# Optimization experiments

Hardware: AMD Instinct MI355X
Metric: run time of the kernel (lower is better)

The kernel has to match this reference:

```python
import jax, jax.numpy as jnp
import numpy as np

EPS = 1e-5


def layer_norm(x, g, b):
    mu = jnp.mean(x, axis=-1, keepdims=True)
    var = jnp.var(x, axis=-1, keepdims=True)
    return (x - mu) * jax.lax.rsqrt(var + EPS) * g + b


def setup_inputs() -> dict:
    key = jax.random.key(0)
    ks = jax.random.split(key, 10)
    B, N, D, H, DFF = 4, 2048, 384, 6, 2048
    s = lambda fan: 1.0 / np.sqrt(fan)
    return {
        "x": jax.random.normal(ks[0], (B, N, D), dtype=jnp.float32),
        "norm_g": jnp.ones((D,), jnp.float32),
        "norm_b": jnp.zeros((D,), jnp.float32),
        "w_qkv": jax.random.uniform(ks[1], (D, 3 * D), jnp.float32, -s(D), s(D)),
        "b_qkv": jax.random.uniform(ks[2], (3 * D,), jnp.float32, -s(D), s(D)),
        "w1": jax.random.uniform(ks[3], (D, DFF), jnp.float32, -s(D), s(D)),
        "b1": jax.random.uniform(ks[4], (DFF,), jnp.float32, -s(D), s(D)),
        "w2": jax.random.uniform(ks[5], (DFF, D), jnp.float32, -s(DFF), s(DFF)),
        "b2": jax.random.uniform(ks[6], (D,), jnp.float32, -s(DFF), s(DFF)),
    }


def reference(x, norm_g, norm_b, w_qkv, b_qkv, w1, b1, w2, b2):
    H = 6
    B, N, D = x.shape
    hd = D // H
    scale = hd ** -0.5

    # --- attention (pre-norm, shared LayerNorm params) ---
    out = layer_norm(x, norm_g, norm_b)
    qkv = out @ w_qkv + b_qkv                     # [B, N, 3D]
    q, k, v = jnp.split(qkv, 3, axis=-1)
    to_heads = lambda t: t.reshape(B, N, H, hd).transpose(0, 2, 1, 3)  # b h n d
    q, k, v = to_heads(q), to_heads(k), to_heads(v)
    scores = jnp.einsum('bhid,bhjd->bhij', q, k) * scale
    attn = jax.nn.softmax(scores, axis=-1)        # dropout is identity in eval
    att = jnp.einsum('bhij,bhjd->bhid', attn, v)  # [B, H, N, hd]
    att = att.transpose(0, 2, 1, 3).reshape(B, N, D)
    x2 = x + att

    # --- MLP (same shared LayerNorm) ---
    y = layer_norm(x2, norm_g, norm_b)
    h = jax.nn.gelu(y @ w1 + b1, approximate=False)  # torch F.gelu exact
    mlp = h @ w2 + b2
    return x2 + mlp
```

## Files before the change

### kernel.cpp

```cpp
#include <hip/hip_runtime.h>
#include <cstdint>
#include <cstddef>

#define DEV static __device__ __forceinline__

typedef __attribute__((ext_vector_type(8))) short short8;
typedef __attribute__((ext_vector_type(4))) float f32x4;
typedef __attribute__((ext_vector_type(4))) unsigned short u16x4;
typedef __attribute__((ext_vector_type(2))) unsigned short u16x2;

constexpr int kB = 4, kN = 2048, kD = 384, kH = 6, kDFF = 2048;
constexpr int kM = kB * kN;
constexpr int kBH = kB * kH;
constexpr float kQPre = 0.18033688011112042f;

DEV float exp2fast(float f) { return __builtin_amdgcn_exp2f(f); }

DEV unsigned short f2b(float f) {
  union { float fp; uint32_t u; } v; v.fp = f;
  return (unsigned short)((v.u + 0x7fffu + ((v.u >> 16) & 1u)) >> 16);
}

DEV void gload16(const unsigned short* g, unsigned short* l) {
  __builtin_amdgcn_global_load_lds(
      (const __attribute__((address_space(1))) unsigned int*)g,
      (__attribute__((address_space(3))) unsigned int*)l, 16, 0, 0);
}

DEV float gelu_fast(float x) {
  float t = exp2fast(x * (2.3022081f + 0.1029432f * x * x));
  return x - x * __builtin_amdgcn_rcpf(t + 1.0f);
}

__global__ __launch_bounds__(256) void k_transpose3(
    const float* __restrict__ wqkv, unsigned short* __restrict__ wqkvT,
    const float* __restrict__ w1,   unsigned short* __restrict__ w1T,
    const float* __restrict__ w2,   unsigned short* __restrict__ w2T) {
  __shared__ unsigned short t[64][66];
  int idx = blockIdx.x;
  const float* w; unsigned short* wT; int K, Nn, nbk;
  if (idx < 108)      { w = wqkv; wT = wqkvT; K = 384;  Nn = 1152; nbk = 6; }
  else if (idx < 300) { w = w1;   wT = w1T;   K = 384;  Nn = 2048; nbk = 6;  idx -= 108; }
  else                { w = w2;   wT = w2T;   K = 2048; Nn = 384;  nbk = 32; idx -= 300; }
  const int bk = idx % nbk, bn = idx / nbk;
  const int k0 = bk << 6, n0 = bn << 6;
  const int tid = threadIdx.x;
  const int cl = tid & 63, rw = tid >> 6;
#pragma unroll
  for (int it = 0; it < 16; ++it) {
    int kk = it * 4 + rw;
    t[cl][kk] = f2b(w[(size_t)(k0 + kk) * Nn + n0 + cl]);
  }
  __syncthreads();
  const int kq = (tid & 15) << 2;
  const int nr = tid >> 4;
#pragma unroll
  for (int it = 0; it < 4; ++it) {
    int nn = it * 16 + nr;
    u16x4 v;
    v[0] = t[nn][kq]; v[1] = t[nn][kq + 1]; v[2] = t[nn][kq + 2]; v[3] = t[nn][kq + 3];
    *(u16x4*)&wT[(size_t)(n0 + nn) * K + k0 + kq] = v;
  }
}

__global__ __launch_bounds__(256) void k_layernorm(
    const float* __restrict__ x, const float* __restrict__ g,
    const float* __restrict__ bta, unsigned short* __restrict__ y) {
  int row  = blockIdx.x * 4 + (threadIdx.x >> 6);
  int lane = threadIdx.x & 63;
  const float* xr = x + (size_t)row * kD;
  float4 a = *(const float4*)(xr + lane * 4);
  float2 c = *(const float2*)(xr + 256 + lane * 2);
  float s  = a.x + a.y + a.z + a.w + c.x + c.y;
  float ss = a.x*a.x + a.y*a.y + a.z*a.z + a.w*a.w + c.x*c.x + c.y*c.y;
#pragma unroll
  for (int m = 1; m < 64; m <<= 1) {
    s  += __shfl_xor(s,  m, 64);
    ss += __shfl_xor(ss, m, 64);
  }
  float mean = s * (1.0f / kD);
  float var  = ss * (1.0f / kD) - mean * mean;
  float r = rsqrtf(var + 1e-5f);
  float4 g4 = *(const float4*)(g + lane * 4);
  float2 g2 = *(const float2*)(g + 256 + lane * 2);
  float4 b4 = *(const float4*)(bta + lane * 4);
  float2 b2 = *(const float2*)(bta + 256 + lane * 2);
  unsigned short* yr = y + (size_t)row * kD;
  u16x4 o4;
  o4[0] = f2b((a.x - mean) * r * g4.x + b4.x);
  o4[1] = f2b((a.y - mean) * r * g4.y + b4.y);
  o4[2] = f2b((a.z - mean) * r * g4.z + b4.z);
  o4[3] = f2b((a.w - mean) * r * g4.w + b4.w);
  *(u16x4*)(yr + lane * 4) = o4;
  u16x2 o2;
  o2[0] = f2b((c.x - mean) * r * g2.x + b2.x);
  o2[1] = f2b((c.y - mean) * r * g2.y + b2.y);
  *(u16x2*)(yr + 256 + lane * 2) = o2;
}

template <int MODE, int TM>
__global__ __launch_bounds__(256) void k_gemm(
    const unsigned short* __restrict__ A, const unsigned short* __restrict__ Bt,
    const float* __restrict__ bias, int K, int Nn, int nbm,
    unsigned short* __restrict__ oq, unsigned short* __restrict__ okk,
    unsigned short* __restrict__ ov, unsigned short* __restrict__ oh,
    const float* __restrict__ res, float* __restrict__ out) {
  constexpr int MI = (TM + 31) / 32;
  __shared__ unsigned short lA[2][TM * 32];
  __shared__ unsigned short lB[2][128 * 32];
  const int tid = threadIdx.x, wid = tid >> 6, lane = tid & 63;
  const int bm = blockIdx.x % nbm, bn = blockIdx.x / nbm;
  const int m0 = bm * TM, n0 = bn * 128;
  const int wr = wid >> 1, wc = wid & 1;
  const int wmo = wr * (TM >> 1);
  const int lr16 = lane & 15, lq = lane >> 4;
  const int gsw = ((lr16 >> 1) & 3) << 3;

  f32x4 acc[MI][4];
#pragma unroll
  for (int i = 0; i < MI; i++)
#pragma unroll
    for (int j = 0; j < 4; j++) acc[i][j] = f32x4{0.f, 0.f, 0.f, 0.f};

  const int srow = (lane >> 2);
  const int scc  = (lane & 3) << 3;

  auto stage = [&](int buf, int k0) {
    if constexpr (TM >= 64) {
#pragma unroll
      for (int p = 0; p < TM / 64; p++) {
        int row = ((wid + (p << 2)) << 4) + srow;
        int sl  = ((lane & 3) ^ ((row >> 1) & 3)) << 3;
        gload16(A + (size_t)(m0 + row) * K + k0 + sl, &lA[buf][(row << 5) + scc]);
      }
    } else {
      if (tid < TM * 4) {
        int row = tid >> 2;
        int sl  = ((tid & 3) ^ ((row >> 1) & 3)) << 3;
        gload16(A + (size_t)(m0 + row) * K + k0 + sl,
                &lA[buf][(row << 5) + ((tid & 3) << 3)]);
      }
    }
#pragma unroll
    for (int p = 0; p < 2; p++) {
      int row = ((wid + (p << 2)) << 4) + srow;
      int sl  = ((lane & 3) ^ ((row >> 1) & 3)) << 3;
      gload16(Bt + (size_t)(n0 + row) * K + k0 + sl, &lB[buf][(row << 5) + scc]);
    }
  };

  stage(0, 0);

  const int nkt = K >> 5;
  for (int kt = 0; kt < nkt; ++kt) {
    const int cur = kt & 1;
    __syncthreads();
    if (kt + 1 < nkt) stage(cur ^ 1, (kt + 1) << 5);
    short8 af[MI], bf[4];
#pragma unroll
    for (int i = 0; i < MI; i++)
      af[i] = *(const short8*)&lA[cur][(wmo + (i << 4) + lr16) * 32 + ((lq << 3) ^ gsw)];
#pragma unroll
    for (int j = 0; j < 4; j++)
      bf[j] = *(const short8*)&lB[cur][((wc << 6) + (j << 4) + lr16) * 32 + ((lq << 3) ^ gsw)];
#pragma unroll
    for (int i = 0; i < MI; i++)
#pragma unroll
      for (int j = 0; j < 4; j++)
        acc[i][j] = __builtin_amdgcn_mfma_f32_16x16x32_bf16(af[i], bf[j], acc[i][j], 0, 0, 0);
  }

#pragma unroll
  for (int i = 0; i < MI; i++) {
    int mbase = m0 + wmo + (i << 4) + (lq << 2);
#pragma unroll
    for (int j = 0; j < 4; j++) {
      int col = n0 + (wc << 6) + (j << 4) + lr16;
      float bv = bias[col];
#pragma unroll
      for (int rr = 0; rr < 4; ++rr) {
        float cvl = acc[i][j][rr] + bv;
        int m = mbase + rr;
        if (MODE == 0) {
          int bI = m >> 11, nI = m & 2047;
          if (col < 384) {
            int hh = col >> 6, dd = col & 63;
            oq[(((size_t)bI * kH + hh) * kN + nI) * 64 + dd] = f2b(cvl * kQPre);
          } else if (col < 768) {
            int c2 = col - 384; int hh = c2 >> 6, dd = c2 & 63;
            okk[(((size_t)bI * kH + hh) * kN + nI) * 64 + dd] = f2b(cvl);
          } else {
            int c2 = col - 768; int hh = c2 >> 6, dd = c2 & 63;
            ov[(((size_t)bI * kH + hh) * 64 + dd) * kN + nI] = f2b(cvl);
          }
        } else if (MODE == 1) {
          oh[(size_t)m * kDFF + col] = f2b(gelu_fast(cvl));
        } else {
          size_t idx = (size_t)m * kD + col;
          out[idx] = res[idx] + cvl;
        }
      }
    }
  }
}

__global__ __launch_bounds__(256) void k_attn(
    const unsigned short* __restrict__ Q, const unsigned short* __restrict__ Kg,
    const unsigned short* __restrict__ Vt, const float* __restrict__ x,
    float* __restrict__ x2) {
  __shared__ unsigned short lK[2][64 * 64];
  __shared__ unsigned short lV[2][64 * 64];
  __shared__ unsigned short lP[4][16 * 64];
  const int tid = threadIdx.x, wid = tid >> 6, lane = tid & 63;
  const int swz = (blockIdx.x & 7) * (gridDim.x >> 3) + (blockIdx.x >> 3);
  const int bh = swz >> 5, qt = swz & 31;
  const int b = bh / kH, h = bh - b * kH;
  const unsigned short* Qp = Q  + (size_t)bh * kN * 64;
  const unsigned short* Kp = Kg + (size_t)bh * kN * 64;
  const unsigned short* Vp = Vt + (size_t)bh * 64 * kN;
  const int lr16 = lane & 15, lq = lane >> 4;
  const int q0w = qt * 64 + wid * 16;
  const int rsw = (lr16 & 7) << 3;

  const int sr  = ((wid << 3) + (lane >> 3));
  const int scc = (lane & 7) << 3;

  short8 qf[2];
#pragma unroll
  for (int ks = 0; ks < 2; ++ks)
    qf[ks] = *(const short8*)(Qp + (size_t)(q0w + lr16) * 64 + ks * 32 + lq * 8);

  const short8 ones = {0x3F80, 0x3F80, 0x3F80, 0x3F80, 0x3F80, 0x3F80, 0x3F80, 0x3F80};
  f32x4 o[4], o_l;
#pragma unroll
  for (int df = 0; df < 4; ++df) o[df] = f32x4{0.f, 0.f, 0.f, 0.f};
  o_l = f32x4{0.f, 0.f, 0.f, 0.f};

  auto stage = [&](int buf, int t) {
#pragma unroll
    for (int p = 0; p < 2; p++) {
      int r = sr + (p << 5);
      int sl = ((lane & 7) ^ (r & 7)) << 3;
      gload16(Kp + (size_t)(t * 64 + r) * 64 + sl, &lK[buf][(r << 6) + scc]);
      gload16(Vp + (size_t)r * kN + t * 64 + sl,   &lV[buf][(r << 6) + scc]);
    }
  };

  stage(0, 0);

  constexpr int kNT = kN / 64;
  for (int t = 0; t < kNT; ++t) {
    const int cur = t & 1;
    __syncthreads();
    if (t + 1 < kNT) stage(cur ^ 1, t + 1);

    f32x4 s4[4];
#pragma unroll
    for (int j = 0; j < 4; j++) {
      s4[j] = f32x4{0.f, 0.f, 0.f, 0.f};
#pragma unroll
      for (int ks = 0; ks < 2; ks++) {
        short8 kf = *(const short8*)&lK[cur][((j << 4) + lr16) * 64 + ((ks * 32 + (lq << 3)) ^ rsw)];
        s4[j] = __builtin_amdgcn_mfma_f32_16x16x32_bf16(kf, qf[ks], s4[j], 0, 0, 0);
      }
    }

#pragma unroll
    for (int j = 0; j < 4; j++) {
      float p0 = exp2fast(s4[j][0]);
      float p1 = exp2fast(s4[j][1]);
      float p2 = exp2fast(s4[j][2]);
      float p3 = exp2fast(s4[j][3]);
      uint32_t w0, w1;
      asm("v_cvt_pk_bf16_f32 %0, %1, %2" : "=v"(w0) : "v"(p0), "v"(p1));
      asm("v_cvt_pk_bf16_f32 %0, %1, %2" : "=v"(w1) : "v"(p2), "v"(p3));
      int kvb = (j << 4) + (lq << 2);
      uint2 wv; wv.x = w0; wv.y = w1;
      *(uint2*)&lP[wid][(lr16 << 6) + (kvb ^ rsw)] = wv;
    }

    short8 pa[2];
#pragma unroll
    for (int ks = 0; ks < 2; ks++)
      pa[ks] = *(const short8*)&lP[wid][(lr16 << 6) + ((ks * 32 + (lq << 3)) ^ rsw)];
#pragma unroll
    for (int ks = 0; ks < 2; ks++)
      o_l = __builtin_amdgcn_mfma_f32_16x16x32_bf16(pa[ks], ones, o_l, 0, 0, 0);
#pragma unroll
    for (int df = 0; df < 4; df++) {
#pragma unroll
      for (int ks = 0; ks < 2; ks++) {
        short8 vf = *(const short8*)&lV[cur][((df << 4) + lr16) * 64 + ((ks * 32 + (lq << 3)) ^ rsw)];
        o[df] = __builtin_amdgcn_mfma_f32_16x16x32_bf16(pa[ks], vf, o[df], 0, 0, 0);
      }
    }
  }

  float inv[4];
#pragma unroll
  for (int rr = 0; rr < 4; rr++) inv[rr] = __builtin_amdgcn_rcpf(o_l[rr]);
#pragma unroll
  for (int df = 0; df < 4; df++)
#pragma unroll
    for (int rr = 0; rr < 4; rr++) {
      int row  = q0w + (lq << 2) + rr;
      int colD = h * 64 + (df << 4) + lr16;
      size_t idx = ((size_t)(b * kN + row)) * kD + colD;
      x2[idx] = x[idx] + o[df][rr] * inv[rr];
    }
}

extern "C" void kernel_launch(void* const* d_in, const int* in_sizes, int n_in,
                              void* d_out, int out_size, void* d_ws, size_t ws_size,
                              hipStream_t stream) {
  const float* x    = (const float*)d_in[0];
  const float* ng   = (const float*)d_in[1];
  const float* nb   = (const float*)d_in[2];
  const float* wqkv = (const float*)d_in[3];
  const float* bqkv = (const float*)d_in[4];
  const float* w1   = (const float*)d_in[5];
  const float* b1   = (const float*)d_in[6];
  const float* w2   = (const float*)d_in[7];
  const float* b2   = (const float*)d_in[8];
  float* out = (float*)d_out;

  char* p = (char*)d_ws;
  auto take = [&](size_t bytes) -> char* {
    char* r = p; p += (bytes + 255) & ~(size_t)255; return r;
  };
  unsigned short* y     = (unsigned short*)take((size_t)kM * kD * 2);
  unsigned short* wqkvT = (unsigned short*)take((size_t)3 * kD * kD * 2);
  unsigned short* w1T   = (unsigned short*)take((size_t)kDFF * kD * 2);
  unsigned short* w2T   = (unsigned short*)take((size_t)kD * kDFF * 2);
  unsigned short* Qw    = (unsigned short*)take((size_t)kM * kD * 2);
  unsigned short* Kw    = (unsigned short*)take((size_t)kM * kD * 2);
  unsigned short* Vtw   = (unsigned short*)take((size_t)kM * kD * 2);
  float*          x2    = (float*)take((size_t)kM * kD * 4);
  unsigned short* hbuf  = (unsigned short*)take((size_t)kM * kDFF * 2);

  k_transpose3<<<492, 256, 0, stream>>>(wqkv, wqkvT, w1, w1T, w2, w2T);

  k_layernorm<<<kM / 4, 256, 0, stream>>>(x, ng, nb, y);
  k_gemm<0, 64><<<128 * 9, 256, 0, stream>>>(y, wqkvT, bqkv, kD, 3 * kD, 128,
                                             Qw, Kw, Vtw, nullptr, nullptr, nullptr);
  k_attn<<<kBH * 32, 256, 0, stream>>>(Qw, Kw, Vtw, x, x2);
  k_layernorm<<<kM / 4, 256, 0, stream>>>(x2, ng, nb, y);
  k_gemm<1, 128><<<64 * 16, 256, 0, stream>>>(y, w1T, b1, kD, kDFF, 64,
                                              nullptr, nullptr, nullptr, hbuf, nullptr, nullptr);
  k_gemm<2, 32><<<256 * 3, 256, 0, stream>>>(hbuf, w2T, b2, kDFF, kD, 256,
                                             nullptr, nullptr, nullptr, nullptr, x2, out);
}
```

Measured before the change: 153.6 us.

## Switch GEMMs to 32x32x16 MFMA and fuse first layernorm into weight-prep kernel

The GEMM kernel now uses 32x32x16 bf16 MFMA tiles with f32x16 accumulators instead of 16x16x32. This cuts LDS fragment loads per MFMA and the instruction count, and the output mapping is rewritten to match. Separately, the first layernorm is folded into the weight-transpose launch as extra blocks, removing one kernel launch and letting the two independent jobs overlap. The risks are higher register pressure and a changed epilogue store pattern, and for TM=32 the per-wave work split changes to four column slices.

```diff
diff --git a/kernel.cpp b/kernel.cpp
--- a/kernel.cpp
+++ b/kernel.cpp
@@ -6,6 +6,7 @@
 
 typedef __attribute__((ext_vector_type(8))) short short8;
 typedef __attribute__((ext_vector_type(4))) float f32x4;
+typedef __attribute__((ext_vector_type(16))) float f32x16;
 typedef __attribute__((ext_vector_type(4))) unsigned short u16x4;
 typedef __attribute__((ext_vector_type(2))) unsigned short u16x2;
 
@@ -32,10 +33,46 @@
   return x - x * __builtin_amdgcn_rcpf(t + 1.0f);
 }
 
-__global__ __launch_bounds__(256) void k_transpose3(
+__global__ __launch_bounds__(256) void k_pre(
     const float* __restrict__ wqkv, unsigned short* __restrict__ wqkvT,
     const float* __restrict__ w1,   unsigned short* __restrict__ w1T,
-    const float* __restrict__ w2,   unsigned short* __restrict__ w2T) {
+    const float* __restrict__ w2,   unsigned short* __restrict__ w2T,
+    const float* __restrict__ x, const float* __restrict__ g,
+    const float* __restrict__ bta, unsigned short* __restrict__ y) {
+  const int tid = threadIdx.x;
+  if (blockIdx.x >= 492) {
+    int row  = (blockIdx.x - 492) * 4 + (tid >> 6);
+    int lane = tid & 63;
+    const float* xr = x + (size_t)row * kD;
+    float4 a = *(const float4*)(xr + lane * 4);
+    float2 c = *(const float2*)(xr + 256 + lane * 2);
+    float s  = a.x + a.y + a.z + a.w + c.x + c.y;
+    float ss = a.x*a.x + a.y*a.y + a.z*a.z + a.w*a.w + c.x*c.x + c.y*c.y;
+#pragma unroll
+    for (int m = 1; m < 64; m <<= 1) {
+      s  += __shfl_xor(s,  m, 64);
+      ss += __shfl_xor(ss, m, 64);
+    }
+    float mean = s * (1.0f / kD);
+    float var  = ss * (1.0f / kD) - mean * mean;
+    float r = rsqrtf(var + 1e-5f);
+    float4 g4 = *(const float4*)(g + lane * 4);
+    float2 g2 = *(const float2*)(g + 256 + lane * 2);
+    float4 b4 = *(const float4*)(bta + lane * 4);
+    float2 b2 = *(const float2*)(bta + 256 + lane * 2);
+    unsigned short* yr = y + (size_t)row * kD;
+    u16x4 o4;
+    o4[0] = f2b((a.x - mean) * r * g4.x + b4.x);
+    o4[1] = f2b((a.y - mean) * r * g4.y + b4.y);
+    o4[2] = f2b((a.z - mean) * r * g4.z + b4.z);
+    o4[3] = f2b((a.w - mean) * r * g4.w + b4.w);
+    *(u16x4*)(yr + lane * 4) = o4;
+    u16x2 o2;
+    o2[0] = f2b((c.x - mean) * r * g2.x + b2.x);
+    o2[1] = f2b((c.y - mean) * r * g2.y + b2.y);
+    *(u16x2*)(yr + 256 + lane * 2) = o2;
+    return;
+  }
   __shared__ unsigned short t[64][66];
   int idx = blockIdx.x;
   const float* w; unsigned short* wT; int K, Nn, nbk;
@@ -44,7 +81,6 @@
   else                { w = w2;   wT = w2T;   K = 2048; Nn = 384;  nbk = 32; idx -= 300; }
   const int bk = idx % nbk, bn = idx / nbk;
   const int k0 = bk << 6, n0 = bn << 6;
-  const int tid = threadIdx.x;
   const int cl = tid & 63, rw = tid >> 6;
 #pragma unroll
   for (int it = 0; it < 16; ++it) {
@@ -105,22 +141,27 @@
     unsigned short* __restrict__ oq, unsigned short* __restrict__ okk,
     unsigned short* __restrict__ ov, unsigned short* __restrict__ oh,
     const float* __restrict__ res, float* __restrict__ out) {
-  constexpr int MI = (TM + 31) / 32;
+  constexpr int FI = (TM >= 64) ? TM / 64 : 1;
+  constexpr int FJ = (TM >= 64) ? 2 : 1;
   __shared__ unsigned short lA[2][TM * 32];
   __shared__ unsigned short lB[2][128 * 32];
   const int tid = threadIdx.x, wid = tid >> 6, lane = tid & 63;
   const int bm = blockIdx.x % nbm, bn = blockIdx.x / nbm;
   const int m0 = bm * TM, n0 = bn * 128;
-  const int wr = wid >> 1, wc = wid & 1;
+  const int wr = (TM >= 64) ? (wid >> 1) : 0;
+  const int wc = (TM >= 64) ? (wid & 1) : wid;
   const int wmo = wr * (TM >> 1);
-  const int lr16 = lane & 15, lq = lane >> 4;
-  const int gsw = ((lr16 >> 1) & 3) << 3;
-
-  f32x4 acc[MI][4];
-#pragma unroll
-  for (int i = 0; i < MI; i++)
-#pragma unroll
-    for (int j = 0; j < 4; j++) acc[i][j] = f32x4{0.f, 0.f, 0.f, 0.f};
+  const int wno = wc * (FJ * 32);
+  const int l31 = lane & 31, lh = lane >> 5;
+  const int gsw = (l31 >> 1) & 3;
+
+  f32x16 acc[FI][FJ];
+#pragma unroll
+  for (int i = 0; i < FI; i++)
+#pragma unroll
+    for (int j = 0; j < FJ; j++)
+#pragma unroll
+      for (int r = 0; r < 16; r++) acc[i][j][r] = 0.f;
 
   const int srow = (lane >> 2);
   const int scc  = (lane & 3) << 3;
@@ -156,31 +197,39 @@
     const int cur = kt & 1;
     __syncthreads();
     if (kt + 1 < nkt) stage(cur ^ 1, (kt + 1) << 5);
-    short8 af[MI], bf[4];
-#pragma unroll
-    for (int i = 0; i < MI; i++)
-      af[i] = *(const short8*)&lA[cur][(wmo + (i << 4) + lr16) * 32 + ((lq << 3) ^ gsw)];
-#pragma unroll
-    for (int j = 0; j < 4; j++)
-      bf[j] = *(const short8*)&lB[cur][((wc << 6) + (j << 4) + lr16) * 32 + ((lq << 3) ^ gsw)];
-#pragma unroll
-    for (int i = 0; i < MI; i++)
-#pragma unroll
-      for (int j = 0; j < 4; j++)
-        acc[i][j] = __builtin_amdgcn_mfma_f32_16x16x32_bf16(af[i], bf[j], acc[i][j], 0, 0, 0);
-  }
-
-#pragma unroll
-  for (int i = 0; i < MI; i++) {
-    int mbase = m0 + wmo + (i << 4) + (lq << 2);
-#pragma unroll
-    for (int j = 0; j < 4; j++) {
-      int col = n0 + (wc << 6) + (j << 4) + lr16;
+    short8 af[FI][2], bf[FJ][2];
+#pragma unroll
+    for (int i = 0; i < FI; i++)
+#pragma unroll
+      for (int ks = 0; ks < 2; ks++)
+        af[i][ks] = *(const short8*)&lA[cur][(wmo + (i << 5) + l31) * 32 +
+                                            ((((ks << 1) + lh) ^ gsw) << 3)];
+#pragma unroll
+    for (int j = 0; j < FJ; j++)
+#pragma unroll
+      for (int ks = 0; ks < 2; ks++)
+        bf[j][ks] = *(const short8*)&lB[cur][(wno + (j << 5) + l31) * 32 +
+                                            ((((ks << 1) + lh) ^ gsw) << 3)];
+#pragma unroll
+    for (int i = 0; i < FI; i++)
+#pragma unroll
+      for (int j = 0; j < FJ; j++)
+#pragma unroll
+        for (int ks = 0; ks < 2; ks++)
+          acc[i][j] = __builtin_amdgcn_mfma_f32_32x32x16_bf16(af[i][ks], bf[j][ks],
+                                                              acc[i][j], 0, 0, 0);
+  }
+
+#pragma unroll
+  for (int i = 0; i < FI; i++) {
+#pragma unroll
+    for (int j = 0; j < FJ; j++) {
+      int col = n0 + wno + (j << 5) + l31;
       float bv = bias[col];
 #pragma unroll
-      for (int rr = 0; rr < 4; ++rr) {
-        float cvl = acc[i][j][rr] + bv;
-        int m = mbase + rr;
+      for (int reg = 0; reg < 16; ++reg) {
+        int m = m0 + wmo + (i << 5) + (reg & 3) + ((reg >> 2) << 3) + (lh << 2);
+        float cvl = acc[i][j][reg] + bv;
         if (MODE == 0) {
           int bI = m >> 11, nI = m & 2047;
           if (col < 384) {
@@ -338,9 +387,8 @@
   float*          x2    = (float*)take((size_t)kM * kD * 4);
   unsigned short* hbuf  = (unsigned short*)take((size_t)kM * kDFF * 2);
 
-  k_transpose3<<<492, 256, 0, stream>>>(wqkv, wqkvT, w1, w1T, w2, w2T);
-
-  k_layernorm<<<kM / 4, 256, 0, stream>>>(x, ng, nb, y);
+  k_pre<<<492 + kM / 4, 256, 0, stream>>>(wqkv, wqkvT, w1, w1T, w2, w2T,
+                                          x, ng, nb, y);
   k_gemm<0, 64><<<128 * 9, 256, 0, stream>>>(y, wqkvT, bqkv, kD, 3 * kD, 128,
                                              Qw, Kw, Vtw, nullptr, nullptr, nullptr);
   k_attn<<<kBH * 32, 256, 0, stream>>>(Qw, Kw, Vtw, x, x2);
```

Result: faster. 150.6 us (-2.0%).
